# Optimization experiments

Measured on AMD Instinct MI355X. Metric: run time of the kernel, lower is better.

Reference implementation:

```python
import jax, jax.numpy as jnp
import numpy as np

EMBED = 512
HEADS = 8
EPS = 1e-5


def setup_inputs() -> dict:
    key = jax.random.key(0)
    ks = jax.random.split(key, 8)
    B, Sq, Skv, D = 4, 2048, 2048, EMBED
    return {
        "layer_input": jax.random.normal(ks[0], (B, Sq, D), jnp.float32),
        "cross_attn_input": jax.random.normal(ks[1], (B, Skv, D), jnp.float32),
        "Wq": jax.random.normal(ks[2], (D, D), jnp.float32) * (D ** -0.5),
        "bq": jnp.zeros((D,), jnp.float32),
        "Wkv": jax.random.normal(ks[3], (D, 2 * D), jnp.float32) * (D ** -0.5),
        "bkv": jnp.zeros((2 * D,), jnp.float32),
        "Wo": jax.random.normal(ks[4], (D, D), jnp.float32) * (D ** -0.5),
        "bo": jnp.zeros((D,), jnp.float32),
        "gamma": jnp.ones((D,), jnp.float32),
        "beta": jnp.zeros((D,), jnp.float32),
    }


def _split_heads(x):
    # ... s (h d) -> ... h s d
    *lead, s, hd = x.shape
    d = hd // HEADS
    return jnp.moveaxis(x.reshape(*lead, s, HEADS, d), -2, -3)


def _merge_heads(x):
    # ... h s d -> ... s (h d)
    x = jnp.moveaxis(x, -3, -2)
    *lead, s, h, d = x.shape
    return x.reshape(*lead, s, h * d)


def reference(layer_input, cross_attn_input, Wq, bq, Wkv, bkv, Wo, bo, gamma, beta):
    scale = (EMBED // HEADS) ** -0.5
    res = layer_input
    q = layer_input @ Wq + bq
    kv = cross_attn_input @ Wkv + bkv
    k, v = jnp.split(kv, 2, axis=-1)
    q, k, v = map(_split_heads, (q, k, v))  # [B, H, S, d]
    scores = jnp.einsum('bhqc,bhkc->bhqk', q, k) * scale
    weights = jax.nn.softmax(scores, axis=-1)  # dropout p=0 -> identity
    out = jnp.einsum('bhqk,bhkc->bhqc', weights, v)
    out = _merge_heads(out)
    out = out @ Wo + bo
    x = out + res
    mu = jnp.mean(x, axis=-1, keepdims=True)
    var = jnp.mean(jnp.square(x - mu), axis=-1, keepdims=True)
    return (x - mu) * jax.lax.rsqrt(var + EPS) * gamma + beta
```

## Files before the change

kernel.cpp:

```cpp
#include <hip/hip_runtime.h>
#include <hip/hip_bf16.h>
#include <stdint.h>

#define SEQ    2048
#define DM     512
#define NHEAD  8
#define HD     64
#define BATCH  4
#define MTOT   (BATCH*SEQ)

typedef __attribute__((ext_vector_type(4))) float  f32x4;
typedef __attribute__((ext_vector_type(8))) short  bf16x8;
typedef __attribute__((ext_vector_type(8))) unsigned short u16x8;
typedef __attribute__((ext_vector_type(4))) unsigned short u16x4;
typedef __attribute__((ext_vector_type(4))) float  fl4;
typedef __attribute__((ext_vector_type(2))) unsigned u32x2;
typedef __attribute__((ext_vector_type(4))) unsigned u32x4;

__device__ __forceinline__ unsigned short f2bf(float f) {
  union { float f; unsigned u; } c; c.f = f;
  return (unsigned short)((c.u + 0x7fffu + ((c.u >> 16) & 1u)) >> 16);
}

__device__ __forceinline__ float bf2f(unsigned short s) {
  unsigned u = (unsigned)s << 16;
  float f; __builtin_memcpy(&f, &u, 4);
  return f;
}

__device__ __forceinline__ void load_lds16(const void* g, void* l) {
  __builtin_amdgcn_global_load_lds((__attribute__((address_space(1))) void*)g,
                                   (__attribute__((address_space(3))) void*)l,
                                   16, 0, 0);
}

__device__ __forceinline__ u32x2 ds_tr16(const void* p) {
  u32x2 r;
  asm volatile("ds_read_b64_tr_b16 %0, %1"
               : "=v"(r)
               : "v"((__attribute__((address_space(3))) const void*)p));
  return r;
}

__device__ __forceinline__ unsigned pack_bf2(float lo, float hi) {
  __hip_bfloat162 h2 = __float22bfloat162_rn(float2{lo, hi});
  unsigned u; __builtin_memcpy(&u, &h2, 4);
  return u;
}

__global__ void k_pre(const float* __restrict__ X, unsigned short* __restrict__ Xb,
                      const float* __restrict__ C, unsigned short* __restrict__ Cb,
                      const float* __restrict__ Wq, unsigned short* __restrict__ Wqt,
                      const float* __restrict__ Wkv, unsigned short* __restrict__ Wkvt,
                      const float* __restrict__ Wo, unsigned short* __restrict__ Wot) {
  __shared__ __align__(16) unsigned short t[64][66];
  int bid = blockIdx.x, tid = threadIdx.x;
  if (bid < 8192) {
    const float* src = (bid < 4096) ? X : C;
    unsigned short* dst = (bid < 4096) ? Xb : Cb;
    int i = (bid & 4095) * 256 + tid;
    fl4 v = *(const fl4*)(src + (size_t)i * 4);
    u32x2 o;
    o[0] = pack_bf2(v[0], v[1]);
    o[1] = pack_bf2(v[2], v[3]);
    *(u32x2*)((void*)(dst + (size_t)i * 4)) = o;
    return;
  }
  int tjob = bid - 8192;
  const float* W; unsigned short* Wt; int Nd, bx, by;
  if (tjob < 64)       { W = Wq;  Wt = Wqt;  Nd = 512;  bx = tjob & 7;  by = tjob >> 3; }
  else if (tjob < 192) { int u = tjob - 64;  W = Wkv; Wt = Wkvt; Nd = 1024; bx = u & 15; by = u >> 4; }
  else                 { int u = tjob - 192; W = Wo;  Wt = Wot;  Nd = 512;  bx = u & 7;  by = u >> 3; }
  int k0 = by * 64, n0 = bx * 64;
  int r = tid >> 2, cs = (tid & 3) * 16;
  const float* src = W + (size_t)(k0 + r) * Nd + n0 + cs;
#pragma unroll
  for (int i = 0; i < 4; ++i) {
    fl4 v = *(const fl4*)(src + i * 4);
    *(unsigned*)&t[r][cs + i*4]     = pack_bf2(v[0], v[1]);
    *(unsigned*)&t[r][cs + i*4 + 2] = pack_bf2(v[2], v[3]);
  }
  __syncthreads();
  unsigned short* drow = Wt + (size_t)(n0 + r) * 512 + k0 + cs;
#pragma unroll
  for (int half = 0; half < 2; ++half) {
    u16x8 o;
#pragma unroll
    for (int i = 0; i < 8; ++i) o[i] = t[cs + half*8 + i][r];
    *(u16x8*)(drow + half * 8) = o;
  }
}

template<int RESID>
__device__ __forceinline__ void gemm128x64(
    const unsigned short* __restrict__ A,
    const unsigned short* __restrict__ Bt,
    const float* __restrict__ bias,
    const unsigned short* __restrict__ res,
    unsigned short* __restrict__ Cout,
    int N, int K, int m0, int n0, float osc,
    unsigned short* Als, unsigned short* Bls) {
  int tid  = threadIdx.x;
  int lane = tid & 63, wave = tid >> 6;
  int q = lane & 15, lk = lane >> 4;
  f32x4 acc[2][4];
#pragma unroll
  for (int mt = 0; mt < 2; ++mt)
#pragma unroll
    for (int nt = 0; nt < 4; ++nt) acc[mt][nt] = f32x4{0.f,0.f,0.f,0.f};

  const unsigned short* gA[4];
#pragma unroll
  for (int it = 0; it < 4; ++it) {
    int idx = tid + it * 256;
    int row = idx >> 3, ch = idx & 7, sc = ch ^ (row & 7);
    gA[it] = A + (size_t)(m0 + row) * K + sc * 8;
  }
  const unsigned short* gB[2];
#pragma unroll
  for (int it = 0; it < 2; ++it) {
    int idx = tid + it * 256;
    int row = idx >> 3, ch = idx & 7, sc = ch ^ (row & 7);
    gB[it] = Bt + (size_t)(n0 + row) * K + sc * 8;
  }
  char* aD = (char*)Als + tid * 16;
  char* bD = (char*)Bls + tid * 16;

#pragma unroll
  for (int it = 0; it < 4; ++it) { load_lds16(gA[it], aD + it * 4096); gA[it] += 64; }
#pragma unroll
  for (int it = 0; it < 2; ++it) { load_lds16(gB[it], bD + it * 4096); gB[it] += 64; }
  __syncthreads();

  int nkb = K >> 6;
  int buf = 0;
  for (int kb = 0; kb < nkb; ++kb) {
    if (kb + 1 < nkb) {
      char* aN = aD + (buf ^ 1) * 16384;
      char* bN = bD + (buf ^ 1) * 8192;
#pragma unroll
      for (int it = 0; it < 4; ++it) { load_lds16(gA[it], aN + it * 4096); gA[it] += 64; }
#pragma unroll
      for (int it = 0; it < 2; ++it) { load_lds16(gB[it], bN + it * 4096); gB[it] += 64; }
    }
    const char* aR = (const char*)Als + buf * 16384;
    const char* bR = (const char*)Bls + buf * 8192;
#pragma unroll
    for (int ks = 0; ks < 2; ++ks) {
      bf16x8 a[2], b[4];
#pragma unroll
      for (int mt = 0; mt < 2; ++mt) {
        int row = wave * 32 + mt * 16 + q;
        a[mt] = *(const bf16x8*)(aR + row * 128 + (((ks*4 + lk) ^ (row & 7)) * 16));
      }
#pragma unroll
      for (int nt = 0; nt < 4; ++nt) {
        int row = nt * 16 + q;
        b[nt] = *(const bf16x8*)(bR + row * 128 + (((ks*4 + lk) ^ (row & 7)) * 16));
      }
#pragma unroll
      for (int mt = 0; mt < 2; ++mt)
#pragma unroll
        for (int nt = 0; nt < 4; ++nt)
          acc[mt][nt] = __builtin_amdgcn_mfma_f32_16x16x32_bf16(a[mt], b[nt], acc[mt][nt], 0, 0, 0);
    }
    __syncthreads();
    buf ^= 1;
  }
#pragma unroll
  for (int nt = 0; nt < 4; ++nt) {
    int col = n0 + nt * 16 + q;
    float bv = bias[col];
#pragma unroll
    for (int mt = 0; mt < 2; ++mt) {
      int rowb = m0 + wave * 32 + mt * 16 + lk * 4;
#pragma unroll
      for (int rr = 0; rr < 4; ++rr) {
        float v = acc[mt][nt][rr] + bv;
        size_t off = (size_t)(rowb + rr) * N + col;
        if (RESID) Cout[off] = f2bf(v + bf2f(res[off]));
        else       Cout[off] = f2bf(v * osc);
      }
    }
  }
}

__global__ __launch_bounds__(256, 3)
void k_projmm(const unsigned short* __restrict__ Xb, const unsigned short* __restrict__ Cb,
              const unsigned short* __restrict__ Wqt, const unsigned short* __restrict__ Wkvt,
              const float* __restrict__ bq, const float* __restrict__ bkv,
              unsigned short* __restrict__ Qb, unsigned short* __restrict__ KVb) {
  __shared__ __align__(16) unsigned short Als[2 * 128 * 64];
  __shared__ __align__(16) unsigned short Bls[2 * 64 * 64];
  int bid = blockIdx.x;
  int l = (bid & 7) * 192 + (bid >> 3);
  const float c1 = 0.125f * 1.44269504088896340736f;
  if (l < 512) {
    int m = l >> 3, n = l & 7;
    gemm128x64<0>(Xb, Wqt, bq, nullptr, Qb, 512, 512, m * 128, n * 64, c1, Als, Bls);
  } else {
    int l2 = l - 512;
    int m = l2 >> 4, n = l2 & 15;
    gemm128x64<0>(Cb, Wkvt, bkv, nullptr, KVb, 1024, 512, m * 128, n * 64, 1.0f, Als, Bls);
  }
}

__global__ __launch_bounds__(256, 3)
void k_omm(const unsigned short* __restrict__ Abuf, const unsigned short* __restrict__ Wot,
           const float* __restrict__ bo, const unsigned short* __restrict__ residb,
           unsigned short* __restrict__ tmp) {
  __shared__ __align__(16) unsigned short Als[2 * 128 * 64];
  __shared__ __align__(16) unsigned short Bls[2 * 64 * 64];
  int bid = blockIdx.x;
  int l = (bid & 7) * 64 + (bid >> 3);
  int m = l >> 3, n = l & 7;
  gemm128x64<1>(Abuf, Wot, bo, residb, tmp, 512, 512, m * 128, n * 64, 1.0f, Als, Bls);
}

__global__ __launch_bounds__(256, 4)
void k_attn(const unsigned short* __restrict__ Qb,
            const unsigned short* __restrict__ KVb,
            unsigned short* __restrict__ Ab) {
  __shared__ __align__(16) unsigned short Klds[2][64 * 64];
  __shared__ __align__(16) unsigned short Vlds[3][4096];
  int tid  = threadIdx.x;
  int lane = tid & 63;
  int q    = lane & 15, lk = lane >> 4;
  int bid = blockIdx.x;
  int swz = (bid & 7) * 128 + (bid >> 3);
  int qt = swz & 31, bh = swz >> 5;
  int b  = bh >> 3, h = bh & 7;
  int q0 = qt * 64 + (tid >> 6) * 16;
  const size_t kvbase = (size_t)b * SEQ * 1024;

  bf16x8 qf0, qf1;
  {
    size_t qrow = (size_t)b * SEQ + q0 + q;
    qf0 = *(const bf16x8*)(Qb + qrow * DM + h * HD + lk * 8);
    qf1 = *(const bf16x8*)(Qb + qrow * DM + h * HD + 32 + lk * 8);
  }
  f32x4 acc[4];
#pragma unroll
  for (int i = 0; i < 4; ++i) acc[i] = f32x4{0.f,0.f,0.f,0.f};
  float l = 0.f;
  u32x4 pbA[2];

  const unsigned short *gK0, *gK1, *gV0, *gV1;
  {
    int r0 = tid >> 3, s0_ = (tid & 7) ^ (r0 & 7);
    gK0 = KVb + kvbase + (size_t)r0 * 1024 + h * HD + s0_ * 8;
    int i1 = tid + 256, r1 = i1 >> 3, s1_ = (i1 & 7) ^ (r1 & 7);
    gK1 = KVb + kvbase + (size_t)r1 * 1024 + h * HD + s1_ * 8;
    int dt0 = tid >> 7, w0 = tid & 127, p0 = w0 >> 1, c80 = (w0 & 1) * 8;
    int t0 = (p0 & 32) + (((p0 >> 2) & 3) << 3) + (((p0 >> 4) & 1) << 2) + (p0 & 3);
    gV0 = KVb + kvbase + (size_t)t0 * 1024 + 512 + h * HD + dt0 * 16 + c80;
    int i1v = tid + 256, dt1 = i1v >> 7, w1 = i1v & 127, p1 = w1 >> 1, c81 = (w1 & 1) * 8;
    int t1 = (p1 & 32) + (((p1 >> 2) & 3) << 3) + (((p1 >> 4) & 1) << 2) + (p1 & 3);
    gV1 = KVb + kvbase + (size_t)t1 * 1024 + 512 + h * HD + dt1 * 16 + c81;
  }
  char* kw0 = (char*)Klds[0] + tid * 16;
  char* kw1 = (char*)Klds[1] + tid * 16;
  char* vw0 = (char*)Vlds[0] + tid * 16;
  char* vw1 = (char*)Vlds[1] + tid * 16;
  char* vw2 = (char*)Vlds[2] + tid * 16;
  const char* kr0 = (const char*)Klds[0];
  const char* kr1 = (const char*)Klds[1];
  const char* vr0 = (const char*)Vlds[0] + lane * 8;
  const char* vr1 = (const char*)Vlds[1] + lane * 8;
  const char* vr2 = (const char*)Vlds[2] + lane * 8;

#define STAGE(kd_, vd_) do {                        \
    load_lds16(gK0, (kd_));                         \
    load_lds16(gK1, (kd_) + 4096);                  \
    load_lds16(gV0, (vd_));                         \
    load_lds16(gV1, (vd_) + 4096);                  \
    gK0 += 65536; gK1 += 65536;                     \
    gV0 += 65536; gV1 += 65536;                     \
  } while (0)

#define ABODY(DO_PV, DO_STAGE, kdst_, vdst_, krd_, vprd_) do {               \
    if (DO_STAGE) STAGE(kdst_, vdst_);                                       \
    if (DO_PV) {                                                             \
      u32x2 tr[2][4][2];                                                     \
      _Pragma("unroll")                                                      \
      for (int ks2 = 0; ks2 < 2; ++ks2)                                      \
        _Pragma("unroll")                                                    \
        for (int dt = 0; dt < 4; ++dt)                                       \
          _Pragma("unroll")                                                  \
          for (int u = 0; u < 2; ++u)                                        \
            tr[ks2][dt][u] = ds_tr16((vprd_) + dt * 2048 + ks2 * 1024 + u * 512); \
      asm volatile("s_waitcnt lgkmcnt(8)" ::: "memory");                     \
      __builtin_amdgcn_sched_barrier(0);                                     \
      __builtin_amdgcn_s_setprio(1);                                         \
      {                                                                      \
        union { u32x4 u; bf16x8 v; } pb;                                     \
        pb.u = pbA[0];                                                       \
        _Pragma("unroll")                                                    \
        for (int dt = 0; dt < 4; ++dt) {                                     \
          union { u32x4 u; bf16x8 v; } cv;                                   \
          cv.u[0] = tr[0][dt][0][0]; cv.u[1] = tr[0][dt][0][1];              \
          cv.u[2] = tr[0][dt][1][0]; cv.u[3] = tr[0][dt][1][1];              \
          acc[dt] = __builtin_amdgcn_mfma_f32_16x16x32_bf16(cv.v, pb.v, acc[dt], 0, 0, 0); \
        }                                                                    \
      }                                                                      \
      asm volatile("s_waitcnt lgkmcnt(0)" ::: "memory");                     \
      __builtin_amdgcn_sched_barrier(0);                                     \
      {                                                                      \
        union { u32x4 u; bf16x8 v; } pb;                                     \
        pb.u = pbA[1];                                                       \
        _Pragma("unroll")                                                    \
        for (int dt = 0; dt < 4; ++dt) {                                     \
          union { u32x4 u; bf16x8 v; } cv;                                   \
          cv.u[0] = tr[1][dt][0][0]; cv.u[1] = tr[1][dt][0][1];              \
          cv.u[2] = tr[1][dt][1][0]; cv.u[3] = tr[1][dt][1][1];              \
          acc[dt] = __builtin_amdgcn_mfma_f32_16x16x32_bf16(cv.v, pb.v, acc[dt], 0, 0, 0); \
        }                                                                    \
      }                                                                      \
      __builtin_amdgcn_s_setprio(0);                                         \
    }                                                                        \
    f32x4 st[4];                                                             \
    _Pragma("unroll")                                                        \
    for (int kt = 0; kt < 4; ++kt) st[kt] = f32x4{0.f,0.f,0.f,0.f};          \
    __builtin_amdgcn_s_setprio(1);                                           \
    _Pragma("unroll")                                                        \
    for (int kt = 0; kt < 4; ++kt) {                                         \
      int row = kt * 16 + q;                                                 \
      bf16x8 kf0 = *(const bf16x8*)((krd_) + row * 128 + ((lk ^ (row & 7)) * 16)); \
      bf16x8 kf1 = *(const bf16x8*)((krd_) + row * 128 + (((4 + lk) ^ (row & 7)) * 16)); \
      st[kt] = __builtin_amdgcn_mfma_f32_16x16x32_bf16(kf0, qf0, st[kt], 0, 0, 0); \
      st[kt] = __builtin_amdgcn_mfma_f32_16x16x32_bf16(kf1, qf1, st[kt], 0, 0, 0); \
    }                                                                        \
    __builtin_amdgcn_s_setprio(0);                                           \
    float p[4][4];                                                           \
    _Pragma("unroll")                                                        \
    for (int kt = 0; kt < 4; ++kt)                                           \
      _Pragma("unroll")                                                      \
      for (int r = 0; r < 4; ++r) {                                          \
        float pe = __builtin_amdgcn_exp2f(st[kt][r]);                        \
        p[kt][r] = pe;                                                       \
        l += pe;                                                             \
      }                                                                      \
    _Pragma("unroll")                                                        \
    for (int ks2 = 0; ks2 < 2; ++ks2) {                                      \
      unsigned u0 = pack_bf2(p[2*ks2][0],     p[2*ks2][1]);                  \
      unsigned u1 = pack_bf2(p[2*ks2][2],     p[2*ks2][3]);                  \
      unsigned u2 = pack_bf2(p[2*ks2 + 1][0], p[2*ks2 + 1][1]);              \
      unsigned u3 = pack_bf2(p[2*ks2 + 1][2], p[2*ks2 + 1][3]);              \
      asm("v_permlane32_swap_b32 %0, %1" : "+v"(u0), "+v"(u2));              \
      asm("v_permlane32_swap_b32 %0, %1" : "+v"(u1), "+v"(u3));              \
      asm("v_permlane16_swap_b32 %0, %1" : "+v"(u0), "+v"(u2));              \
      asm("v_permlane16_swap_b32 %0, %1" : "+v"(u1), "+v"(u3));              \
      pbA[ks2][0] = u0; pbA[ks2][1] = u1;                                    \
      pbA[ks2][2] = u2; pbA[ks2][3] = u3;                                    \
    }                                                                        \
    __syncthreads();                                                         \
  } while (0)

  STAGE(kw0, vw0);
  __syncthreads();

  ABODY(0, 1, kw1, vw1, kr0, vr0);
  for (int g = 0; g < 5; ++g) {
    ABODY(1, 1, kw0, vw2, kr1, vr0);
    ABODY(1, 1, kw1, vw0, kr0, vr1);
    ABODY(1, 1, kw0, vw1, kr1, vr2);
    ABODY(1, 1, kw1, vw2, kr0, vr0);
    ABODY(1, 1, kw0, vw0, kr1, vr1);
    ABODY(1, 1, kw1, vw1, kr0, vr2);
  }
  ABODY(1, 0, kw0, vw0, kr1, vr0);

  {
    u32x2 tr[2][4][2];
#pragma unroll
    for (int ks2 = 0; ks2 < 2; ++ks2)
#pragma unroll
      for (int dt = 0; dt < 4; ++dt)
#pragma unroll
        for (int u = 0; u < 2; ++u)
          tr[ks2][dt][u] = ds_tr16(vr1 + dt * 2048 + ks2 * 1024 + u * 512);
    asm volatile("s_waitcnt lgkmcnt(0)" ::: "memory");
    __builtin_amdgcn_sched_barrier(0);
#pragma unroll
    for (int ks2 = 0; ks2 < 2; ++ks2) {
      union { u32x4 u; bf16x8 v; } pb;
      pb.u = pbA[ks2];
#pragma unroll
      for (int dt = 0; dt < 4; ++dt) {
        union { u32x4 u; bf16x8 v; } cv;
        cv.u[0] = tr[ks2][dt][0][0]; cv.u[1] = tr[ks2][dt][0][1];
        cv.u[2] = tr[ks2][dt][1][0]; cv.u[3] = tr[ks2][dt][1][1];
        acc[dt] = __builtin_amdgcn_mfma_f32_16x16x32_bf16(cv.v, pb.v, acc[dt], 0, 0, 0);
      }
    }
  }

  l += __shfl_xor(l, 16);
  l += __shfl_xor(l, 32);
  float inv = 1.0f / l;
  size_t orow = ((size_t)b * SEQ + q0 + q) * DM + h * HD + lk * 4;
#pragma unroll
  for (int dt = 0; dt < 4; ++dt) {
    u16x4 o;
#pragma unroll
    for (int r = 0; r < 4; ++r) o[r] = f2bf(acc[dt][r] * inv);
    *(u16x4*)(Ab + orow + dt * 16) = o;
  }
#undef STAGE
#undef ABODY
}

__global__ void k_ln(const unsigned short* __restrict__ x, const float* __restrict__ gamma,
                     const float* __restrict__ beta, float* __restrict__ out) {
  int tid = threadIdx.x, lane = tid & 63, wave = tid >> 6;
  size_t row = (size_t)blockIdx.x * 4 + wave;
  u16x8 xv = *(const u16x8*)(x + row * DM + lane * 8);
  float v[8];
#pragma unroll
  for (int i = 0; i < 8; ++i) v[i] = bf2f(xv[i]);
  float s  = (v[0]+v[1]) + (v[2]+v[3]) + (v[4]+v[5]) + (v[6]+v[7]);
  float ss = (v[0]*v[0]+v[1]*v[1]) + (v[2]*v[2]+v[3]*v[3])
           + (v[4]*v[4]+v[5]*v[5]) + (v[6]*v[6]+v[7]*v[7]);
#pragma unroll
  for (int off = 1; off < 64; off <<= 1) {
    s  += __shfl_xor(s, off);
    ss += __shfl_xor(ss, off);
  }
  float mu  = s * (1.0f / DM);
  float var = ss * (1.0f / DM) - mu * mu;
  float w = rsqrtf(var + 1e-5f);
  fl4 g0 = *(const fl4*)(gamma + lane*8), g1 = *(const fl4*)(gamma + lane*8 + 4);
  fl4 b0 = *(const fl4*)(beta + lane*8),  b1 = *(const fl4*)(beta + lane*8 + 4);
  fl4 o0, o1;
#pragma unroll
  for (int i = 0; i < 4; ++i) {
    o0[i] = (v[i]     - mu) * w * g0[i] + b0[i];
    o1[i] = (v[4 + i] - mu) * w * g1[i] + b1[i];
  }
  float* orow = out + row * DM + lane * 8;
  *(fl4*)orow = o0;
  *(fl4*)(orow + 4) = o1;
}

extern "C" void kernel_launch(void* const* d_in, const int* in_sizes, int n_in,
                              void* d_out, int out_size, void* d_ws, size_t ws_size,
                              hipStream_t stream) {
  const float* layer_input = (const float*)d_in[0];
  const float* cross       = (const float*)d_in[1];
  const float* Wq   = (const float*)d_in[2];
  const float* bq   = (const float*)d_in[3];
  const float* Wkv  = (const float*)d_in[4];
  const float* bkv  = (const float*)d_in[5];
  const float* Wo   = (const float*)d_in[6];
  const float* bo   = (const float*)d_in[7];
  const float* gamma = (const float*)d_in[8];
  const float* beta  = (const float*)d_in[9];
  float* out = (float*)d_out;

  char* ws = (char*)d_ws;
  unsigned short* Xb   = (unsigned short*)(ws + (size_t)0);
  unsigned short* Cb   = (unsigned short*)(ws + ((size_t)8  << 20));
  unsigned short* Qb   = (unsigned short*)(ws + ((size_t)16 << 20));
  unsigned short* KVb  = (unsigned short*)(ws + ((size_t)24 << 20));
  unsigned short* Abuf = (unsigned short*)(ws + ((size_t)40 << 20));
  unsigned short* tmpb = (unsigned short*)(ws + ((size_t)48 << 20));
  unsigned short* Wqt  = (unsigned short*)(ws + ((size_t)64 << 20));
  unsigned short* Wkvt = (unsigned short*)(ws + ((size_t)65 << 20));
  unsigned short* Wot  = (unsigned short*)(ws + ((size_t)67 << 20));

  k_pre<<<8448, 256, 0, stream>>>(layer_input, Xb, cross, Cb,
                                  Wq, Wqt, Wkv, Wkvt, Wo, Wot);
  k_projmm<<<1536, 256, 0, stream>>>(Xb, Cb, Wqt, Wkvt, bq, bkv, Qb, KVb);
  k_attn<<<1024, 256, 0, stream>>>(Qb, KVb, Abuf);
  k_omm<<<512, 256, 0, stream>>>(Abuf, Wot, bo, Xb, tmpb);
  k_ln<<<MTOT/4, 256, 0, stream>>>(tmpb, gamma, beta, out);
}
```

Measured before the change: 107.6 us.

## Triple-buffer K tiles and use vmcnt-counted barriers in attention loop

Adds a third LDS buffer for K so K tiles are prefetched two iterations ahead while V stays one ahead. The full __syncthreads after each iteration is replaced by an s_waitcnt vmcnt(N) plus s_barrier, so outstanding global-to-LDS loads for later tiles can stay in flight across the barrier. The aim is to hide memory latency better in the attention inner loop. In exchange LDS use grows and launch bounds drop from 4 to 3 blocks per CU, which lowers occupancy.

```diff
diff --git a/kernel.cpp b/kernel.cpp
--- a/kernel.cpp
+++ b/kernel.cpp
@@ -217,11 +217,11 @@
   gemm128x64<1>(Abuf, Wot, bo, residb, tmp, 512, 512, m * 128, n * 64, 1.0f, Als, Bls);
 }
 
-__global__ __launch_bounds__(256, 4)
+__global__ __launch_bounds__(256, 3)
 void k_attn(const unsigned short* __restrict__ Qb,
             const unsigned short* __restrict__ KVb,
             unsigned short* __restrict__ Ab) {
-  __shared__ __align__(16) unsigned short Klds[2][64 * 64];
+  __shared__ __align__(16) unsigned short Klds[3][4096];
   __shared__ __align__(16) unsigned short Vlds[3][4096];
   int tid  = threadIdx.x;
   int lane = tid & 63;
@@ -260,26 +260,36 @@
   }
   char* kw0 = (char*)Klds[0] + tid * 16;
   char* kw1 = (char*)Klds[1] + tid * 16;
+  char* kw2 = (char*)Klds[2] + tid * 16;
   char* vw0 = (char*)Vlds[0] + tid * 16;
   char* vw1 = (char*)Vlds[1] + tid * 16;
   char* vw2 = (char*)Vlds[2] + tid * 16;
   const char* kr0 = (const char*)Klds[0];
   const char* kr1 = (const char*)Klds[1];
+  const char* kr2 = (const char*)Klds[2];
   const char* vr0 = (const char*)Vlds[0] + lane * 8;
   const char* vr1 = (const char*)Vlds[1] + lane * 8;
   const char* vr2 = (const char*)Vlds[2] + lane * 8;
 
-#define STAGE(kd_, vd_) do {                        \
+#define STAGE_VT(vd_) do {                          \
+    load_lds16(gV0, (vd_));                         \
+    load_lds16(gV1, (vd_) + 4096);                  \
+    gV0 += 65536; gV1 += 65536;                     \
+  } while (0)
+#define STAGE_KT(kd_) do {                          \
     load_lds16(gK0, (kd_));                         \
     load_lds16(gK1, (kd_) + 4096);                  \
-    load_lds16(gV0, (vd_));                         \
-    load_lds16(gV1, (vd_) + 4096);                  \
     gK0 += 65536; gK1 += 65536;                     \
-    gV0 += 65536; gV1 += 65536;                     \
   } while (0)
-
-#define ABODY(DO_PV, DO_STAGE, kdst_, vdst_, krd_, vprd_) do {               \
-    if (DO_STAGE) STAGE(kdst_, vdst_);                                       \
+#define VMCNT_BARRIER(N) do {                                        \
+    asm volatile("s_waitcnt vmcnt(" #N ")" ::: "memory");            \
+    __builtin_amdgcn_sched_barrier(0);                               \
+    __builtin_amdgcn_s_barrier();                                    \
+  } while (0)
+
+#define ABODY(DO_PV, SV, SK, WAITN, kdst_, vdst_, krd_, vprd_) do {          \
+    if (SV) STAGE_VT(vdst_);                                                 \
+    if (SK) STAGE_KT(kdst_);                                                 \
     if (DO_PV) {                                                             \
       u32x2 tr[2][4][2];                                                     \
       _Pragma("unroll")                                                      \
@@ -353,22 +363,24 @@
       pbA[ks2][0] = u0; pbA[ks2][1] = u1;                                    \
       pbA[ks2][2] = u2; pbA[ks2][3] = u3;                                    \
     }                                                                        \
-    __syncthreads();                                                         \
+    VMCNT_BARRIER(WAITN);                                                    \
   } while (0)
 
-  STAGE(kw0, vw0);
-  __syncthreads();
-
-  ABODY(0, 1, kw1, vw1, kr0, vr0);
-  for (int g = 0; g < 5; ++g) {
-    ABODY(1, 1, kw0, vw2, kr1, vr0);
-    ABODY(1, 1, kw1, vw0, kr0, vr1);
-    ABODY(1, 1, kw0, vw1, kr1, vr2);
-    ABODY(1, 1, kw1, vw2, kr0, vr0);
-    ABODY(1, 1, kw0, vw0, kr1, vr1);
-    ABODY(1, 1, kw1, vw1, kr0, vr2);
-  }
-  ABODY(1, 0, kw0, vw0, kr1, vr0);
+  STAGE_VT(vw0);
+  STAGE_KT(kw0);
+  STAGE_KT(kw1);
+  VMCNT_BARRIER(2);
+
+  ABODY(0, 1, 1, 4, kw2, vw1, kr0, vr0);
+  for (int g = 0; g < 9; ++g) {
+    ABODY(1, 1, 1, 4, kw0, vw2, kr1, vr0);
+    ABODY(1, 1, 1, 4, kw1, vw0, kr2, vr1);
+    ABODY(1, 1, 1, 4, kw2, vw1, kr0, vr2);
+  }
+  ABODY(1, 1, 1, 4, kw0, vw2, kr1, vr0);
+  ABODY(1, 1, 1, 4, kw1, vw0, kr2, vr1);
+  ABODY(1, 1, 0, 2, kw2, vw1, kr0, vr2);
+  ABODY(1, 0, 0, 0, kw0, vw0, kr1, vr0);
 
   {
     u32x2 tr[2][4][2];
@@ -406,7 +418,9 @@
     for (int r = 0; r < 4; ++r) o[r] = f2bf(acc[dt][r] * inv);
     *(u16x4*)(Ab + orow + dt * 16) = o;
   }
-#undef STAGE
+#undef STAGE_VT
+#undef STAGE_KT
+#undef VMCNT_BARRIER
 #undef ABODY
 }
 
```

Result: no change. 109.7 us (+1.9%).

## Write V transposed from projection GEMM epilogue and read it directly in attention

Applied to the files above, without the earlier changes.

The KV projection GEMM now writes the V half in a per-head transposed layout [bh][d][seq], staged through LDS in its epilogue. The attention kernel loads V tiles from that buffer with swizzled 16-byte row reads instead of the transposing ds_read_b64_tr_b16 path and its extra waitcnt scheduling. This removes the per-iteration LDS transpose reads in attention, at the cost of an extra LDS round-trip and store pass in the projection epilogue. The Vt buffer shares its workspace offset with tmpb, which is only written afterwards by k_omm.

```diff
diff --git a/kernel.cpp b/kernel.cpp
--- a/kernel.cpp
+++ b/kernel.cpp
@@ -32,14 +32,6 @@
   __builtin_amdgcn_global_load_lds((__attribute__((address_space(1))) void*)g,
                                    (__attribute__((address_space(3))) void*)l,
                                    16, 0, 0);
-}
-
-__device__ __forceinline__ u32x2 ds_tr16(const void* p) {
-  u32x2 r;
-  asm volatile("ds_read_b64_tr_b16 %0, %1"
-               : "=v"(r)
-               : "v"((__attribute__((address_space(3))) const void*)p));
-  return r;
 }
 
 __device__ __forceinline__ unsigned pack_bf2(float lo, float hi) {
@@ -91,7 +83,7 @@
   }
 }
 
-template<int RESID>
+template<int MODE>
 __device__ __forceinline__ void gemm128x64(
     const unsigned short* __restrict__ A,
     const unsigned short* __restrict__ Bt,
@@ -99,7 +91,8 @@
     const unsigned short* __restrict__ res,
     unsigned short* __restrict__ Cout,
     int N, int K, int m0, int n0, float osc,
-    unsigned short* Als, unsigned short* Bls) {
+    unsigned short* Als, unsigned short* Bls,
+    unsigned short* Vt = nullptr, int bh = 0) {
   int tid  = threadIdx.x;
   int lane = tid & 63, wave = tid >> 6;
   int q = lane & 15, lk = lane >> 4;
@@ -167,6 +160,29 @@
     __syncthreads();
     buf ^= 1;
   }
+  if (MODE == 2) {
+    unsigned short* T = Als;
+#pragma unroll
+    for (int nt = 0; nt < 4; ++nt) {
+      int coll = nt * 16 + q;
+      float bv = bias[n0 + coll];
+#pragma unroll
+      for (int mt = 0; mt < 2; ++mt) {
+        int rowl = wave * 32 + mt * 16 + lk * 4;
+#pragma unroll
+        for (int rr = 0; rr < 4; ++rr)
+          T[coll * 136 + rowl + rr] = f2bf(acc[mt][nt][rr] + bv);
+      }
+    }
+    __syncthreads();
+    int dv = tid >> 2, c = tid & 3;
+    const unsigned short* s = T + dv * 136 + c * 32;
+    unsigned short* d = Vt + ((size_t)bh * 64 + dv) * 2048 + (m0 & 2047) + c * 32;
+#pragma unroll
+    for (int i = 0; i < 4; ++i)
+      *(u16x8*)(d + i * 8) = *(const u16x8*)(s + i * 8);
+    return;
+  }
 #pragma unroll
   for (int nt = 0; nt < 4; ++nt) {
     int col = n0 + nt * 16 + q;
@@ -178,8 +194,8 @@
       for (int rr = 0; rr < 4; ++rr) {
         float v = acc[mt][nt][rr] + bv;
         size_t off = (size_t)(rowb + rr) * N + col;
-        if (RESID) Cout[off] = f2bf(v + bf2f(res[off]));
-        else       Cout[off] = f2bf(v * osc);
+        if (MODE == 1) Cout[off] = f2bf(v + bf2f(res[off]));
+        else           Cout[off] = f2bf(v * osc);
       }
     }
   }
@@ -189,7 +205,8 @@
 void k_projmm(const unsigned short* __restrict__ Xb, const unsigned short* __restrict__ Cb,
               const unsigned short* __restrict__ Wqt, const unsigned short* __restrict__ Wkvt,
               const float* __restrict__ bq, const float* __restrict__ bkv,
-              unsigned short* __restrict__ Qb, unsigned short* __restrict__ KVb) {
+              unsigned short* __restrict__ Qb, unsigned short* __restrict__ KVb,
+              unsigned short* __restrict__ Vt) {
   __shared__ __align__(16) unsigned short Als[2 * 128 * 64];
   __shared__ __align__(16) unsigned short Bls[2 * 64 * 64];
   int bid = blockIdx.x;
@@ -201,7 +218,11 @@
   } else {
     int l2 = l - 512;
     int m = l2 >> 4, n = l2 & 15;
-    gemm128x64<0>(Cb, Wkvt, bkv, nullptr, KVb, 1024, 512, m * 128, n * 64, 1.0f, Als, Bls);
+    if (n < 8)
+      gemm128x64<0>(Cb, Wkvt, bkv, nullptr, KVb, 1024, 512, m * 128, n * 64, 1.0f, Als, Bls);
+    else
+      gemm128x64<2>(Cb, Wkvt, bkv, nullptr, KVb, 1024, 512, m * 128, n * 64, 1.0f, Als, Bls,
+                    Vt, (m >> 4) * 8 + (n - 8));
   }
 }
 
@@ -220,8 +241,9 @@
 __global__ __launch_bounds__(256, 4)
 void k_attn(const unsigned short* __restrict__ Qb,
             const unsigned short* __restrict__ KVb,
+            const unsigned short* __restrict__ Vtg,
             unsigned short* __restrict__ Ab) {
-  __shared__ __align__(16) unsigned short Klds[2][64 * 64];
+  __shared__ __align__(16) unsigned short Klds[2][4096];
   __shared__ __align__(16) unsigned short Vlds[3][4096];
   int tid  = threadIdx.x;
   int lane = tid & 63;
@@ -251,12 +273,8 @@
     gK0 = KVb + kvbase + (size_t)r0 * 1024 + h * HD + s0_ * 8;
     int i1 = tid + 256, r1 = i1 >> 3, s1_ = (i1 & 7) ^ (r1 & 7);
     gK1 = KVb + kvbase + (size_t)r1 * 1024 + h * HD + s1_ * 8;
-    int dt0 = tid >> 7, w0 = tid & 127, p0 = w0 >> 1, c80 = (w0 & 1) * 8;
-    int t0 = (p0 & 32) + (((p0 >> 2) & 3) << 3) + (((p0 >> 4) & 1) << 2) + (p0 & 3);
-    gV0 = KVb + kvbase + (size_t)t0 * 1024 + 512 + h * HD + dt0 * 16 + c80;
-    int i1v = tid + 256, dt1 = i1v >> 7, w1 = i1v & 127, p1 = w1 >> 1, c81 = (w1 & 1) * 8;
-    int t1 = (p1 & 32) + (((p1 >> 2) & 3) << 3) + (((p1 >> 4) & 1) << 2) + (p1 & 3);
-    gV1 = KVb + kvbase + (size_t)t1 * 1024 + 512 + h * HD + dt1 * 16 + c81;
+    gV0 = Vtg + ((size_t)bh * 64 + r0) * 2048 + s0_ * 8;
+    gV1 = Vtg + ((size_t)bh * 64 + r1) * 2048 + s1_ * 8;
   }
   char* kw0 = (char*)Klds[0] + tid * 16;
   char* kw1 = (char*)Klds[1] + tid * 16;
@@ -265,9 +283,9 @@
   char* vw2 = (char*)Vlds[2] + tid * 16;
   const char* kr0 = (const char*)Klds[0];
   const char* kr1 = (const char*)Klds[1];
-  const char* vr0 = (const char*)Vlds[0] + lane * 8;
-  const char* vr1 = (const char*)Vlds[1] + lane * 8;
-  const char* vr2 = (const char*)Vlds[2] + lane * 8;
+  const char* vr0 = (const char*)Vlds[0];
+  const char* vr1 = (const char*)Vlds[1];
+  const char* vr2 = (const char*)Vlds[2];
 
 #define STAGE(kd_, vd_) do {                        \
     load_lds16(gK0, (kd_));                         \
@@ -275,46 +293,30 @@
     load_lds16(gV0, (vd_));                         \
     load_lds16(gV1, (vd_) + 4096);                  \
     gK0 += 65536; gK1 += 65536;                     \
-    gV0 += 65536; gV1 += 65536;                     \
+    gV0 += 64; gV1 += 64;                           \
   } while (0)
 
 #define ABODY(DO_PV, DO_STAGE, kdst_, vdst_, krd_, vprd_) do {               \
     if (DO_STAGE) STAGE(kdst_, vdst_);                                       \
     if (DO_PV) {                                                             \
-      u32x2 tr[2][4][2];                                                     \
+      bf16x8 vf0[4], vf1[4];                                                 \
       _Pragma("unroll")                                                      \
-      for (int ks2 = 0; ks2 < 2; ++ks2)                                      \
-        _Pragma("unroll")                                                    \
-        for (int dt = 0; dt < 4; ++dt)                                       \
-          _Pragma("unroll")                                                  \
-          for (int u = 0; u < 2; ++u)                                        \
-            tr[ks2][dt][u] = ds_tr16((vprd_) + dt * 2048 + ks2 * 1024 + u * 512); \
-      asm volatile("s_waitcnt lgkmcnt(8)" ::: "memory");                     \
-      __builtin_amdgcn_sched_barrier(0);                                     \
+      for (int dt = 0; dt < 4; ++dt) {                                       \
+        int row = dt * 16 + q;                                               \
+        vf0[dt] = *(const bf16x8*)((vprd_) + row * 128 + ((lk ^ (q & 7)) * 16)); \
+        vf1[dt] = *(const bf16x8*)((vprd_) + row * 128 + (((4 + lk) ^ (q & 7)) * 16)); \
+      }                                                                      \
       __builtin_amdgcn_s_setprio(1);                                         \
       {                                                                      \
         union { u32x4 u; bf16x8 v; } pb;                                     \
         pb.u = pbA[0];                                                       \
         _Pragma("unroll")                                                    \
-        for (int dt = 0; dt < 4; ++dt) {                                     \
-          union { u32x4 u; bf16x8 v; } cv;                                   \
-          cv.u[0] = tr[0][dt][0][0]; cv.u[1] = tr[0][dt][0][1];              \
-          cv.u[2] = tr[0][dt][1][0]; cv.u[3] = tr[0][dt][1][1];              \
-          acc[dt] = __builtin_amdgcn_mfma_f32_16x16x32_bf16(cv.v, pb.v, acc[dt], 0, 0, 0); \
-        }                                                                    \
-      }                                                                      \
-      asm volatile("s_waitcnt lgkmcnt(0)" ::: "memory");                     \
-      __builtin_amdgcn_sched_barrier(0);                                     \
-      {                                                                      \
-        union { u32x4 u; bf16x8 v; } pb;                                     \
+        for (int dt = 0; dt < 4; ++dt)                                       \
+          acc[dt] = __builtin_amdgcn_mfma_f32_16x16x32_bf16(vf0[dt], pb.v, acc[dt], 0, 0, 0); \
         pb.u = pbA[1];                                                       \
         _Pragma("unroll")                                                    \
-        for (int dt = 0; dt < 4; ++dt) {                                     \
-          union { u32x4 u; bf16x8 v; } cv;                                   \
-          cv.u[0] = tr[1][dt][0][0]; cv.u[1] = tr[1][dt][0][1];              \
-          cv.u[2] = tr[1][dt][1][0]; cv.u[3] = tr[1][dt][1][1];              \
-          acc[dt] = __builtin_amdgcn_mfma_f32_16x16x32_bf16(cv.v, pb.v, acc[dt], 0, 0, 0); \
-        }                                                                    \
+        for (int dt = 0; dt < 4; ++dt)                                       \
+          acc[dt] = __builtin_amdgcn_mfma_f32_16x16x32_bf16(vf1[dt], pb.v, acc[dt], 0, 0, 0); \
       }                                                                      \
       __builtin_amdgcn_s_setprio(0);                                         \
     }                                                                        \
@@ -325,8 +327,8 @@
     _Pragma("unroll")                                                        \
     for (int kt = 0; kt < 4; ++kt) {                                         \
       int row = kt * 16 + q;                                                 \
-      bf16x8 kf0 = *(const bf16x8*)((krd_) + row * 128 + ((lk ^ (row & 7)) * 16)); \
-      bf16x8 kf1 = *(const bf16x8*)((krd_) + row * 128 + (((4 + lk) ^ (row & 7)) * 16)); \
+      bf16x8 kf0 = *(const bf16x8*)((krd_) + row * 128 + ((lk ^ (q & 7)) * 16)); \
+      bf16x8 kf1 = *(const bf16x8*)((krd_) + row * 128 + (((4 + lk) ^ (q & 7)) * 16)); \
       st[kt] = __builtin_amdgcn_mfma_f32_16x16x32_bf16(kf0, qf0, st[kt], 0, 0, 0); \
       st[kt] = __builtin_amdgcn_mfma_f32_16x16x32_bf16(kf1, qf1, st[kt], 0, 0, 0); \
     }                                                                        \
@@ -371,28 +373,22 @@
   ABODY(1, 0, kw0, vw0, kr1, vr0);
 
   {
-    u32x2 tr[2][4][2];
-#pragma unroll
-    for (int ks2 = 0; ks2 < 2; ++ks2)
-#pragma unroll
-      for (int dt = 0; dt < 4; ++dt)
-#pragma unroll
-        for (int u = 0; u < 2; ++u)
-          tr[ks2][dt][u] = ds_tr16(vr1 + dt * 2048 + ks2 * 1024 + u * 512);
-    asm volatile("s_waitcnt lgkmcnt(0)" ::: "memory");
-    __builtin_amdgcn_sched_barrier(0);
-#pragma unroll
-    for (int ks2 = 0; ks2 < 2; ++ks2) {
-      union { u32x4 u; bf16x8 v; } pb;
-      pb.u = pbA[ks2];
-#pragma unroll
-      for (int dt = 0; dt < 4; ++dt) {
-        union { u32x4 u; bf16x8 v; } cv;
-        cv.u[0] = tr[ks2][dt][0][0]; cv.u[1] = tr[ks2][dt][0][1];
-        cv.u[2] = tr[ks2][dt][1][0]; cv.u[3] = tr[ks2][dt][1][1];
-        acc[dt] = __builtin_amdgcn_mfma_f32_16x16x32_bf16(cv.v, pb.v, acc[dt], 0, 0, 0);
-      }
+    bf16x8 vf0[4], vf1[4];
+#pragma unroll
+    for (int dt = 0; dt < 4; ++dt) {
+      int row = dt * 16 + q;
+      vf0[dt] = *(const bf16x8*)(vr1 + row * 128 + ((lk ^ (q & 7)) * 16));
+      vf1[dt] = *(const bf16x8*)(vr1 + row * 128 + (((4 + lk) ^ (q & 7)) * 16));
     }
+    union { u32x4 u; bf16x8 v; } pb;
+    pb.u = pbA[0];
+#pragma unroll
+    for (int dt = 0; dt < 4; ++dt)
+      acc[dt] = __builtin_amdgcn_mfma_f32_16x16x32_bf16(vf0[dt], pb.v, acc[dt], 0, 0, 0);
+    pb.u = pbA[1];
+#pragma unroll
+    for (int dt = 0; dt < 4; ++dt)
+      acc[dt] = __builtin_amdgcn_mfma_f32_16x16x32_bf16(vf1[dt], pb.v, acc[dt], 0, 0, 0);
   }
 
   l += __shfl_xor(l, 16);
@@ -463,6 +459,7 @@
   unsigned short* Qb   = (unsigned short*)(ws + ((size_t)16 << 20));
   unsigned short* KVb  = (unsigned short*)(ws + ((size_t)24 << 20));
   unsigned short* Abuf = (unsigned short*)(ws + ((size_t)40 << 20));
+  unsigned short* Vt   = (unsigned short*)(ws + ((size_t)48 << 20));
   unsigned short* tmpb = (unsigned short*)(ws + ((size_t)48 << 20));
   unsigned short* Wqt  = (unsigned short*)(ws + ((size_t)64 << 20));
   unsigned short* Wkvt = (unsigned short*)(ws + ((size_t)65 << 20));
@@ -470,8 +467,8 @@
 
   k_pre<<<8448, 256, 0, stream>>>(layer_input, Xb, cross, Cb,
                                   Wq, Wqt, Wkv, Wkvt, Wo, Wot);
-  k_projmm<<<1536, 256, 0, stream>>>(Xb, Cb, Wqt, Wkvt, bq, bkv, Qb, KVb);
-  k_attn<<<1024, 256, 0, stream>>>(Qb, KVb, Abuf);
+  k_projmm<<<1536, 256, 0, stream>>>(Xb, Cb, Wqt, Wkvt, bq, bkv, Qb, KVb, Vt);
+  k_attn<<<1024, 256, 0, stream>>>(Qb, KVb, Vt, Abuf);
   k_omm<<<512, 256, 0, stream>>>(Abuf, Wot, bo, Xb, tmpb);
   k_ln<<<MTOT/4, 256, 0, stream>>>(tmpb, gamma, beta, out);
 }
```

Result: no change. 106.4 us (-1.1%).
